# Kernel optimization log

Measured on AMD Instinct MI355X. Metric: run time of the kernel, lower is better.

Reference implementation:

```python
import jax, jax.numpy as jnp
import numpy as np

NUM_ENTS = 100000
NUM_RELS = 237
IN_CH, OUT_CH, KER = 1, 32, 9
IN_DIM = 200
K = 10
OUT_DIM = K * IN_DIM                      # 2000
L_IN = OUT_DIM // IN_CH                   # 2000
L_OUT = (L_IN - KER) // 1 + 1             # 1992
FC_LEN = OUT_CH * L_OUT                   # 63744
BATCH = 512
EPS = 1e-5


def _bn(x, gamma, beta, axes):
    # training-mode batch norm (biased variance), matching torch BatchNorm1d forward
    m = jnp.mean(x, axis=axes, keepdims=True)
    v = jnp.var(x, axis=axes, keepdims=True)
    return (x - m) * jax.lax.rsqrt(v + EPS) * gamma + beta


def setup_inputs() -> dict:
    key = jax.random.key(0)
    ks = jax.random.split(key, 8)
    xavier = lambda k, shape, fan: jax.random.normal(k, shape, jnp.float32) * np.sqrt(2.0 / fan)
    E = xavier(ks[0], (NUM_ENTS, IN_DIM), NUM_ENTS + IN_DIM)
    R = xavier(ks[1], (NUM_RELS * 2, OUT_CH, IN_CH, KER), OUT_CH * IN_CH * KER)
    e_W = xavier(ks[2], (IN_DIM, OUT_DIM), IN_DIM + OUT_DIM)
    fc_W = xavier(ks[3], (IN_DIM, FC_LEN), IN_DIM + FC_LEN)  # torch Linear weight [out, in]
    return {
        "E": E, "R": R, "e_W": e_W, "fc_W": fc_W,
        "bn0_gamma": jnp.ones((IN_DIM,), jnp.float32), "bn0_beta": jnp.zeros((IN_DIM,), jnp.float32),
        "bn1_gamma": jnp.ones((OUT_CH,), jnp.float32), "bn1_beta": jnp.zeros((OUT_CH,), jnp.float32),
        "bn2_gamma": jnp.ones((IN_DIM,), jnp.float32), "bn2_beta": jnp.zeros((IN_DIM,), jnp.float32),
        "e1_idx": jax.random.randint(ks[4], (BATCH,), 0, NUM_ENTS),
        "r_idx": jax.random.randint(ks[5], (BATCH,), 0, NUM_RELS * 2),
    }


def reference(E, R, e_W, fc_W, bn0_gamma, bn0_beta, bn1_gamma, bn1_beta,
              bn2_gamma, bn2_beta, e1_idx, r_idx):
    B = e1_idx.shape[0]
    x = E[e1_idx]                                   # [B, 200]
    x = _bn(x, bn0_gamma, bn0_beta, axes=0)
    x = x @ e_W                                     # [B, 2000]
    k = R[r_idx]                                    # [B, O, C, KER] per-sample filters
    x = x.reshape(B, IN_CH, L_IN)                   # [B, C, L_in]
    # per-sample grouped conv1d == batched small matmul over sliding windows
    win = jnp.arange(L_OUT)[:, None] + jnp.arange(KER)[None, :]  # [L_out, KER]
    patches = x[:, :, win]                          # [B, C, L_out, KER]
    x = jnp.einsum('bock,bclk->bol', k, patches)    # [B, O, L_out]
    x = _bn(x, bn1_gamma[:, None], bn1_beta[:, None], axes=(0, 2))
    x = x.reshape(B, FC_LEN)
    x = x @ fc_W.T                                  # [B, 200]
    x = jnp.tanh(_bn(x, bn2_gamma, bn2_beta, axes=0))
    logits = x @ E.T                                # [B, num_ents]
    return jax.nn.sigmoid(logits)
```

## Files before the change

kernel.cpp:

```cpp
#include <hip/hip_runtime.h>

#define NENT 100000
#define DIM 200
#define ODIM 2000
#define KERN 9
#define OCH 32
#define LOUT 1992
#define FCLEN 63744
#define BSZ 512
#define EPSV 1e-5f
#define KPAD 224

typedef float f32x4 __attribute__((ext_vector_type(4)));
typedef short short8 __attribute__((ext_vector_type(8)));
typedef __bf16 bf16x8 __attribute__((ext_vector_type(8)));
typedef unsigned int uint4v __attribute__((ext_vector_type(4)));
typedef unsigned int uint2v __attribute__((ext_vector_type(2)));

__device__ __forceinline__ unsigned short f2bf(float f) {
  unsigned int u = __float_as_uint(f);
  return (unsigned short)((u + 0x7fffu + ((u >> 16) & 1u)) >> 16);
}

__device__ __forceinline__ float wredf(float v) {
#pragma unroll
  for (int o = 32; o > 0; o >>= 1) v += __shfl_down(v, o, 64);
  return v;
}

__global__ void k_init(float* bias) {
  int t = threadIdx.x;
  if (t < DIM) bias[t] = 0.f;
}

__global__ void k_bn0(const float* __restrict__ E, const int* __restrict__ e1,
                      const float* __restrict__ g, const float* __restrict__ b,
                      float* __restrict__ A, float* __restrict__ Bc) {
  int f = blockIdx.x, ln = threadIdx.x;
  float s1 = 0.f, s2 = 0.f;
  for (int i = ln; i < BSZ; i += 64) {
    float v = E[(long)e1[i] * DIM + f];
    s1 += v; s2 += v * v;
  }
  s1 = wredf(s1); s2 = wredf(s2);
  if (ln == 0) {
    float m = s1 / BSZ;
    float var = s2 / BSZ - m * m;
    float a = g[f] * rsqrtf(var + EPSV);
    A[f] = a; Bc[f] = b[f] - m * a;
  }
}

__global__ void __launch_bounds__(256) k_mm1(
    const float* __restrict__ E, const int* __restrict__ e1,
    const float* __restrict__ eW, const float* __restrict__ A,
    const float* __restrict__ Bc, float* __restrict__ x1) {
  __shared__ float xs[8][DIM];
  int t = threadIdx.x, b0 = blockIdx.x * 8;
  for (int idx = t; idx < 8 * DIM; idx += 256) {
    int bi = idx / DIM, f = idx % DIM;
    xs[bi][f] = E[(long)e1[b0 + bi] * DIM + f] * A[f] + Bc[f];
  }
  __syncthreads();
  float acc[8][8];
#pragma unroll
  for (int bi = 0; bi < 8; bi++)
#pragma unroll
    for (int m = 0; m < 8; m++) acc[bi][m] = 0.f;
  for (int k = 0; k < DIM; k++) {
    float ew[8];
#pragma unroll
    for (int m = 0; m < 8; m++) {
      int j = t + 256 * m;
      ew[m] = (j < ODIM) ? eW[(long)k * ODIM + j] : 0.f;
    }
#pragma unroll
    for (int bi = 0; bi < 8; bi++) {
      float xv = xs[bi][k];
#pragma unroll
      for (int m = 0; m < 8; m++) acc[bi][m] += xv * ew[m];
    }
  }
#pragma unroll
  for (int bi = 0; bi < 8; bi++)
#pragma unroll
    for (int m = 0; m < 8; m++) {
      int j = t + 256 * m;
      if (j < ODIM) x1[(long)(b0 + bi) * ODIM + j] = acc[bi][m];
    }
}

__global__ void __launch_bounds__(256) k_conv(
    const float* __restrict__ x1, const float* __restrict__ R,
    const int* __restrict__ ridx, unsigned short* __restrict__ convb,
    float* __restrict__ part) {
  __shared__ float xs[ODIM];
  __shared__ float kr[OCH * KERN];
  __shared__ float wr4[4][64];
  int t = threadIdx.x, b = blockIdx.x;
  for (int i = t; i < ODIM; i += 256) xs[i] = x1[(long)b * ODIM + i];
  for (int i = t; i < OCH * KERN; i += 256) kr[i] = R[(long)ridx[b] * (OCH * KERN) + i];
  __syncthreads();
  int l0 = t * 8;
  bool act = (t < 249);
  float w[16];
  if (act) {
#pragma unroll
    for (int i = 0; i < 16; i++) w[i] = xs[l0 + i];
  }
  int wv = t >> 6, ln = t & 63;
  for (int o = 0; o < OCH; o++) {
    float s1 = 0.f, s2 = 0.f;
    if (act) {
      float kk[KERN];
#pragma unroll
      for (int k = 0; k < KERN; k++) kk[k] = kr[o * KERN + k];
      float cb[8];
#pragma unroll
      for (int j = 0; j < 8; j++) {
        float c = 0.f;
#pragma unroll
        for (int k = 0; k < KERN; k++) c += kk[k] * w[j + k];
        cb[j] = c; s1 += c; s2 += c * c;
      }
      uint4v pk;
#pragma unroll
      for (int i = 0; i < 4; i++)
        pk[i] = (unsigned)f2bf(cb[2 * i]) | ((unsigned)f2bf(cb[2 * i + 1]) << 16);
      *(uint4v*)(convb + (long)b * FCLEN + o * LOUT + l0) = pk;
    }
    s1 = wredf(s1); s2 = wredf(s2);
    if (ln == 0) { wr4[wv][o] = s1; wr4[wv][o + 32] = s2; }
  }
  __syncthreads();
  if (t < 64) part[(long)b * 64 + t] = wr4[0][t] + wr4[1][t] + wr4[2][t] + wr4[3][t];
}

__global__ void k_bn1fin(const float* __restrict__ part, const float* __restrict__ g,
                         const float* __restrict__ b, float* __restrict__ a,
                         float* __restrict__ c) {
  __shared__ float sm[4][64];
  __shared__ float tot[64];
  int t = threadIdx.x;
  int si = t >> 6, st = t & 63;
  float s = 0.f;
  for (int i = si; i < BSZ; i += 4) s += part[(long)i * 64 + st];
  sm[si][st] = s;
  __syncthreads();
  if (t < 64) tot[t] = sm[0][t] + sm[1][t] + sm[2][t] + sm[3][t];
  __syncthreads();
  if (t < OCH) {
    float N = (float)BSZ * LOUT;
    float m = tot[t] / N;
    float var = tot[t + 32] / N - m * m;
    float av = g[t] * rsqrtf(var + EPSV);
    a[t] = av; c[t] = b[t] - m * av;
  }
}

__global__ void __launch_bounds__(256) k_fcw(
    const float* __restrict__ fcW, const float* __restrict__ a,
    const float* __restrict__ c, unsigned short* __restrict__ fcWb,
    float* __restrict__ bias) {
  int d = blockIdx.x, o = blockIdx.y, t = threadIdx.x;
  const float* src = fcW + (long)d * FCLEN + o * LOUT;
  unsigned short* dst = fcWb + (long)d * FCLEN + o * LOUT;
  float ao = a[o];
  float s = 0.f;
  if (t < 249) {
    float v[8];
#pragma unroll
    for (int j = 0; j < 8; j++) { v[j] = src[t * 8 + j]; s += v[j]; }
    uint4v pk;
#pragma unroll
    for (int i = 0; i < 4; i++)
      pk[i] = (unsigned)f2bf(v[2 * i] * ao) | ((unsigned)f2bf(v[2 * i + 1] * ao) << 16);
    *(uint4v*)(dst + t * 8) = pk;
  }
  s = wredf(s);
  __shared__ float sm[4];
  if ((t & 63) == 0) sm[t >> 6] = s;
  __syncthreads();
  if (t == 0) atomicAdd(bias + d, c[o] * (sm[0] + sm[1] + sm[2] + sm[3]));
}

__global__ void k_yinit(const float* __restrict__ bias, float* __restrict__ y) {
  int i = blockIdx.x * 256 + threadIdx.x;
  y[i] = bias[i % DIM];
}

__global__ void __launch_bounds__(256) k_gemm_fc(
    const unsigned short* __restrict__ convb, const unsigned short* __restrict__ fcWb,
    float* __restrict__ y) {
  __shared__ unsigned short lA[128 * 104];
  __shared__ unsigned short lB[128 * 104];
  int t = threadIdx.x;
  int b0 = blockIdx.x * 128, n0 = blockIdx.y * 128, z = blockIdx.z;
  int s0 = (664 * z) / 32, s1 = (664 * (z + 1)) / 32;
  int w = t >> 6, lane = t & 63, lm = lane & 15, quad = lane >> 4;
  int mq = (w >> 1) * 64, nq = (w & 1) * 64;
  f32x4 acc[4][4];
#pragma unroll
  for (int mi = 0; mi < 4; mi++)
#pragma unroll
    for (int ni = 0; ni < 4; ni++) acc[mi][ni] = (f32x4){0.f, 0.f, 0.f, 0.f};
  for (int st = s0; st < s1; st++) {
    long kc = (long)st * 96;
    __syncthreads();
#pragma unroll
    for (int i = 0; i < 6; i++) {
      int cc = t + 256 * i;
      int row = cc / 12, c8 = cc % 12;
      *(uint4v*)&lA[row * 104 + c8 * 8] =
          *(const uint4v*)&convb[(long)(b0 + row) * FCLEN + kc + c8 * 8];
      uint4v bv = (uint4v){0u, 0u, 0u, 0u};
      int nr = n0 + row;
      if (nr < DIM) bv = *(const uint4v*)&fcWb[(long)nr * FCLEN + kc + c8 * 8];
      *(uint4v*)&lB[row * 104 + c8 * 8] = bv;
    }
    __syncthreads();
#pragma unroll
    for (int ks = 0; ks < 96; ks += 32) {
      short8 af[4], bfr[4];
#pragma unroll
      for (int i2 = 0; i2 < 4; i2++) {
        af[i2] = *(const short8*)&lA[(mq + i2 * 16 + lm) * 104 + ks + quad * 8];
        bfr[i2] = *(const short8*)&lB[(nq + i2 * 16 + lm) * 104 + ks + quad * 8];
      }
#pragma unroll
      for (int mi = 0; mi < 4; mi++)
#pragma unroll
        for (int ni = 0; ni < 4; ni++)
          acc[mi][ni] = __builtin_amdgcn_mfma_f32_16x16x32_bf16(
              __builtin_bit_cast(bf16x8, af[mi]), __builtin_bit_cast(bf16x8, bfr[ni]),
              acc[mi][ni], 0, 0, 0);
    }
  }
#pragma unroll
  for (int mi = 0; mi < 4; mi++)
#pragma unroll
    for (int ni = 0; ni < 4; ni++)
#pragma unroll
      for (int r = 0; r < 4; r++) {
        int gm = b0 + mq + mi * 16 + quad * 4 + r;
        int gn = n0 + nq + ni * 16 + lm;
        if (gn < DIM) atomicAdd(&y[(long)gm * DIM + gn], acc[mi][ni][r]);
      }
}

__global__ void k_bn2(const float* __restrict__ y, const float* __restrict__ g,
                      const float* __restrict__ b, unsigned short* __restrict__ xt) {
  int d = blockIdx.x, ln = threadIdx.x;
  if (d >= DIM) {
    for (int i = ln; i < BSZ; i += 64) xt[(long)i * KPAD + d] = 0;
    return;
  }
  float v[8];
  float s1 = 0.f, s2 = 0.f;
#pragma unroll
  for (int j = 0; j < 8; j++) {
    v[j] = y[(long)(ln + 64 * j) * DIM + d];
    s1 += v[j]; s2 += v[j] * v[j];
  }
  s1 = wredf(s1); s2 = wredf(s2);
  s1 = __shfl(s1, 0, 64); s2 = __shfl(s2, 0, 64);
  float m = s1 / BSZ, var = s2 / BSZ - m * m;
  float a = g[d] * rsqrtf(var + EPSV), c = b[d] - m * a;
#pragma unroll
  for (int j = 0; j < 8; j++)
    xt[(long)(ln + 64 * j) * KPAD + d] = f2bf(tanhf(v[j] * a + c));
}

__global__ void __launch_bounds__(256) k_gemmf(
    const unsigned short* __restrict__ xt, const float* __restrict__ E,
    float* __restrict__ out) {
  __shared__ unsigned short lB[64 * 232];
  int t = threadIdx.x;
  long e0 = (long)blockIdx.x * 64;
#pragma unroll
  for (int i = 0; i < 13; i++) {
    int cc = t + 256 * i;
    if (cc < 3200) {
      int row = cc / 50, c4 = cc % 50;
      long e = e0 + row;
      f32x4 v = (f32x4){0.f, 0.f, 0.f, 0.f};
      if (e < NENT) v = *(const f32x4*)&E[e * DIM + c4 * 4];
      uint2v pk;
      pk[0] = (unsigned)f2bf(v[0]) | ((unsigned)f2bf(v[1]) << 16);
      pk[1] = (unsigned)f2bf(v[2]) | ((unsigned)f2bf(v[3]) << 16);
      *(uint2v*)&lB[row * 232 + c4 * 4] = pk;
    }
  }
  {
    int row = t >> 2, cp = t & 3;
    uint4v z = (uint4v){0u, 0u, 0u, 0u};
    *(uint4v*)&lB[row * 232 + 200 + cp * 8] = z;
  }
  __syncthreads();
  int w = t >> 6, lane = t & 63, lm = lane & 15, quad = lane >> 4;
  int r0 = w * 128;
  f32x4 acc[8][4];
#pragma unroll
  for (int mi = 0; mi < 8; mi++)
#pragma unroll
    for (int ni = 0; ni < 4; ni++) acc[mi][ni] = (f32x4){0.f, 0.f, 0.f, 0.f};
#pragma unroll
  for (int kk = 0; kk < 7; kk++) {
    int k0 = kk * 32;
    short8 bfr[4];
#pragma unroll
    for (int ni = 0; ni < 4; ni++)
      bfr[ni] = *(const short8*)&lB[(ni * 16 + lm) * 232 + k0 + quad * 8];
#pragma unroll
    for (int mi = 0; mi < 8; mi++) {
      short8 af = *(const short8*)&xt[(long)(r0 + mi * 16 + lm) * KPAD + k0 + quad * 8];
#pragma unroll
      for (int ni = 0; ni < 4; ni++)
        acc[mi][ni] = __builtin_amdgcn_mfma_f32_16x16x32_bf16(
            __builtin_bit_cast(bf16x8, af), __builtin_bit_cast(bf16x8, bfr[ni]),
            acc[mi][ni], 0, 0, 0);
    }
  }
#pragma unroll
  for (int mi = 0; mi < 8; mi++)
#pragma unroll
    for (int ni = 0; ni < 4; ni++)
#pragma unroll
      for (int r = 0; r < 4; r++) {
        int gb = r0 + mi * 16 + quad * 4 + r;
        long ge = e0 + ni * 16 + lm;
        if (ge < NENT) {
          float x = acc[mi][ni][r];
          out[(long)gb * NENT + ge] = 1.f / (1.f + __expf(-x));
        }
      }
}

extern "C" void kernel_launch(void* const* d_in, const int* in_sizes, int n_in,
                              void* d_out, int out_size, void* d_ws, size_t ws_size,
                              hipStream_t stream) {
  const float* E = (const float*)d_in[0];
  const float* R = (const float*)d_in[1];
  const float* eW = (const float*)d_in[2];
  const float* fcW = (const float*)d_in[3];
  const float* bn0g = (const float*)d_in[4];
  const float* bn0b = (const float*)d_in[5];
  const float* bn1g = (const float*)d_in[6];
  const float* bn1b = (const float*)d_in[7];
  const float* bn2g = (const float*)d_in[8];
  const float* bn2b = (const float*)d_in[9];
  const int* e1 = (const int*)d_in[10];
  const int* ridx = (const int*)d_in[11];
  float* outp = (float*)d_out;

  char* p = (char*)d_ws;
  size_t off = 0;
  auto alloc = [&](size_t bytes) -> char* {
    char* r = p + off;
    off = (off + bytes + 255) & ~(size_t)255;
    return r;
  };
  float* x1 = (float*)alloc((size_t)BSZ * ODIM * 4);
  unsigned short* convb = (unsigned short*)alloc((size_t)BSZ * FCLEN * 2);
  unsigned short* fcWb = (unsigned short*)alloc((size_t)DIM * FCLEN * 2);
  float* y = (float*)alloc((size_t)BSZ * DIM * 4);
  unsigned short* xt = (unsigned short*)alloc((size_t)BSZ * KPAD * 2);
  float* bn0A = (float*)alloc(DIM * 4);
  float* bn0B = (float*)alloc(DIM * 4);
  float* part = (float*)alloc((size_t)BSZ * 64 * 4);
  float* bn1a = (float*)alloc(OCH * 4);
  float* bn1c = (float*)alloc(OCH * 4);
  float* bias = (float*)alloc(DIM * 4);

  k_init<<<1, 256, 0, stream>>>(bias);
  k_bn0<<<DIM, 64, 0, stream>>>(E, e1, bn0g, bn0b, bn0A, bn0B);
  k_mm1<<<64, 256, 0, stream>>>(E, e1, eW, bn0A, bn0B, x1);
  k_conv<<<BSZ, 256, 0, stream>>>(x1, R, ridx, convb, part);
  k_bn1fin<<<1, 256, 0, stream>>>(part, bn1g, bn1b, bn1a, bn1c);
  k_fcw<<<dim3(DIM, OCH), 256, 0, stream>>>(fcW, bn1a, bn1c, fcWb, bias);
  k_yinit<<<400, 256, 0, stream>>>(bias, y);
  k_gemm_fc<<<dim3(4, 2, 32), 256, 0, stream>>>(convb, fcWb, y);
  k_bn2<<<KPAD, 64, 0, stream>>>(y, bn2g, bn2b, xt);
  k_gemmf<<<dim3((NENT + 63) / 64), 256, 0, stream>>>(xt, E, outp);
}
```

Measured before the change: 658.8 us.

## Retile first GEMM over more blocks and replace split-K atomics with partial-sum reduction

The e_W projection kernel now runs on a 32x16 grid, each block handling 16 rows by 128 columns, instead of 64 blocks each covering 8 rows and all 2000 columns. This spreads the work over far more blocks so more of the device is busy. The split-K FC GEMM now writes its partial tiles to a 32-slice buffer instead of using atomicAdd into y. A new reduction kernel sums the slices plus the bias, replacing the y-initialisation kernel. This trades atomic contention for an extra 16MB write and read pass over the partial buffer.

```diff
diff --git a/kernel.cpp b/kernel.cpp
--- a/kernel.cpp
+++ b/kernel.cpp
@@ -55,39 +55,42 @@
     const float* __restrict__ E, const int* __restrict__ e1,
     const float* __restrict__ eW, const float* __restrict__ A,
     const float* __restrict__ Bc, float* __restrict__ x1) {
-  __shared__ float xs[8][DIM];
-  int t = threadIdx.x, b0 = blockIdx.x * 8;
-  for (int idx = t; idx < 8 * DIM; idx += 256) {
+  __shared__ float xs[16][DIM];
+  int t = threadIdx.x;
+  int b0 = blockIdx.x * 16, n0 = blockIdx.y * 128;
+  for (int idx = t; idx < 16 * DIM; idx += 256) {
     int bi = idx / DIM, f = idx % DIM;
     xs[bi][f] = E[(long)e1[b0 + bi] * DIM + f] * A[f] + Bc[f];
   }
   __syncthreads();
-  float acc[8][8];
-#pragma unroll
-  for (int bi = 0; bi < 8; bi++)
-#pragma unroll
-    for (int m = 0; m < 8; m++) acc[bi][m] = 0.f;
-  for (int k = 0; k < DIM; k++) {
-    float ew[8];
-#pragma unroll
-    for (int m = 0; m < 8; m++) {
-      int j = t + 256 * m;
-      ew[m] = (j < ODIM) ? eW[(long)k * ODIM + j] : 0.f;
-    }
-#pragma unroll
-    for (int bi = 0; bi < 8; bi++) {
-      float xv = xs[bi][k];
-#pragma unroll
-      for (int m = 0; m < 8; m++) acc[bi][m] += xv * ew[m];
-    }
-  }
-#pragma unroll
-  for (int bi = 0; bi < 8; bi++)
-#pragma unroll
-    for (int m = 0; m < 8; m++) {
-      int j = t + 256 * m;
-      if (j < ODIM) x1[(long)(b0 + bi) * ODIM + j] = acc[bi][m];
-    }
+  int lane = t & 63, w = t >> 6;
+  int j0 = n0 + lane, j1 = j0 + 64;
+  int r0 = w * 4;
+  bool c0 = (j0 < ODIM), c1 = (j1 < ODIM);
+  float acc[4][2];
+#pragma unroll
+  for (int r = 0; r < 4; r++) { acc[r][0] = 0.f; acc[r][1] = 0.f; }
+  for (int k = 0; k < DIM; k += 4) {
+    f32x4 xr[4];
+#pragma unroll
+    for (int r = 0; r < 4; r++) xr[r] = *(const f32x4*)&xs[r0 + r][k];
+#pragma unroll
+    for (int kk = 0; kk < 4; kk++) {
+      float e0v = c0 ? eW[(long)(k + kk) * ODIM + j0] : 0.f;
+      float e1v = c1 ? eW[(long)(k + kk) * ODIM + j1] : 0.f;
+#pragma unroll
+      for (int r = 0; r < 4; r++) {
+        acc[r][0] += xr[r][kk] * e0v;
+        acc[r][1] += xr[r][kk] * e1v;
+      }
+    }
+  }
+#pragma unroll
+  for (int r = 0; r < 4; r++) {
+    long base = (long)(b0 + r0 + r) * ODIM;
+    if (c0) x1[base + j0] = acc[r][0];
+    if (c1) x1[base + j1] = acc[r][1];
+  }
 }
 
 __global__ void __launch_bounds__(256) k_conv(
@@ -184,14 +187,9 @@
   if (t == 0) atomicAdd(bias + d, c[o] * (sm[0] + sm[1] + sm[2] + sm[3]));
 }
 
-__global__ void k_yinit(const float* __restrict__ bias, float* __restrict__ y) {
-  int i = blockIdx.x * 256 + threadIdx.x;
-  y[i] = bias[i % DIM];
-}
-
 __global__ void __launch_bounds__(256) k_gemm_fc(
     const unsigned short* __restrict__ convb, const unsigned short* __restrict__ fcWb,
-    float* __restrict__ y) {
+    float* __restrict__ ypart) {
   __shared__ unsigned short lA[128 * 104];
   __shared__ unsigned short lB[128 * 104];
   int t = threadIdx.x;
@@ -244,8 +242,19 @@
       for (int r = 0; r < 4; r++) {
         int gm = b0 + mq + mi * 16 + quad * 4 + r;
         int gn = n0 + nq + ni * 16 + lm;
-        if (gn < DIM) atomicAdd(&y[(long)gm * DIM + gn], acc[mi][ni][r]);
-      }
+        ypart[((long)z * BSZ + gm) * 256 + gn] = acc[mi][ni][r];
+      }
+}
+
+__global__ void __launch_bounds__(256) k_yred(
+    const float* __restrict__ ypart, const float* __restrict__ bias,
+    float* __restrict__ y) {
+  int i = blockIdx.x * 256 + threadIdx.x;
+  int m = i / DIM, d = i % DIM;
+  float s = bias[d];
+#pragma unroll 8
+  for (int z = 0; z < 32; z++) s += ypart[((long)z * BSZ + m) * 256 + d];
+  y[(long)m * DIM + d] = s;
 }
 
 __global__ void k_bn2(const float* __restrict__ y, const float* __restrict__ g,
@@ -293,8 +302,8 @@
   }
   {
     int row = t >> 2, cp = t & 3;
-    uint4v z = (uint4v){0u, 0u, 0u, 0u};
-    *(uint4v*)&lB[row * 232 + 200 + cp * 8] = z;
+    uint4v zz = (uint4v){0u, 0u, 0u, 0u};
+    *(uint4v*)&lB[row * 232 + 200 + cp * 8] = zz;
   }
   __syncthreads();
   int w = t >> 6, lane = t & 63, lm = lane & 15, quad = lane >> 4;
@@ -363,6 +372,7 @@
   float* x1 = (float*)alloc((size_t)BSZ * ODIM * 4);
   unsigned short* convb = (unsigned short*)alloc((size_t)BSZ * FCLEN * 2);
   unsigned short* fcWb = (unsigned short*)alloc((size_t)DIM * FCLEN * 2);
+  float* ypart = (float*)alloc((size_t)32 * BSZ * 256 * 4);
   float* y = (float*)alloc((size_t)BSZ * DIM * 4);
   unsigned short* xt = (unsigned short*)alloc((size_t)BSZ * KPAD * 2);
   float* bn0A = (float*)alloc(DIM * 4);
@@ -374,12 +384,12 @@
 
   k_init<<<1, 256, 0, stream>>>(bias);
   k_bn0<<<DIM, 64, 0, stream>>>(E, e1, bn0g, bn0b, bn0A, bn0B);
-  k_mm1<<<64, 256, 0, stream>>>(E, e1, eW, bn0A, bn0B, x1);
+  k_mm1<<<dim3(32, 16), 256, 0, stream>>>(E, e1, eW, bn0A, bn0B, x1);
   k_conv<<<BSZ, 256, 0, stream>>>(x1, R, ridx, convb, part);
   k_bn1fin<<<1, 256, 0, stream>>>(part, bn1g, bn1b, bn1a, bn1c);
   k_fcw<<<dim3(DIM, OCH), 256, 0, stream>>>(fcW, bn1a, bn1c, fcWb, bias);
-  k_yinit<<<400, 256, 0, stream>>>(bias, y);
-  k_gemm_fc<<<dim3(4, 2, 32), 256, 0, stream>>>(convb, fcWb, y);
+  k_gemm_fc<<<dim3(4, 2, 32), 256, 0, stream>>>(convb, fcWb, ypart);
+  k_yred<<<400, 256, 0, stream>>>(ypart, bias, y);
   k_bn2<<<KPAD, 64, 0, stream>>>(y, bn2g, bn2b, xt);
   k_gemmf<<<dim3((NENT + 63) / 64), 256, 0, stream>>>(xt, E, outp);
 }
```

Measured after the change: 561.1 us. 14.8% less time.
